# Kernel tuning notes

Hardware: AMD Instinct MI355X
Metric: run time of the kernel (lower is better)

The kernel has to match this reference:

```python
import jax, jax.numpy as jnp
import numpy as np

NEG = jnp.float32(-1e9)
N_PRE = 12000   # n_train_pre_nms (module default training=True)
N_POST = 2000   # n_train_post_nms
MIN_SIZE = 16.0
NMS_THRESH = 0.7


def _make_anchors(feat_size=64, stride=16):
    scales = np.array([128.0, 256.0, 512.0])
    ratios = np.array([0.5, 1.0, 2.0])
    ws = (scales[:, None] * np.sqrt(1.0 / ratios)[None, :]).reshape(-1)  # [9]
    hs = (scales[:, None] * np.sqrt(ratios)[None, :]).reshape(-1)        # [9]
    ctr = (np.arange(feat_size) + 0.5) * stride
    cy, cx = np.meshgrid(ctr, ctr, indexing='ij')
    cx = cx.reshape(-1, 1); cy = cy.reshape(-1, 1)                       # [4096,1]
    x1 = cx - 0.5 * ws[None, :]; y1 = cy - 0.5 * hs[None, :]
    x2 = cx + 0.5 * ws[None, :]; y2 = cy + 0.5 * hs[None, :]
    return np.stack([x1, y1, x2, y2], axis=-1).reshape(-1, 4).astype(np.float32)  # [36864,4]


def setup_inputs() -> dict:
    key = jax.random.key(0)
    k1, k2 = jax.random.split(key)
    anchors = jnp.asarray(_make_anchors())[None]            # [1, 36864, 4]
    B, N = 8, anchors.shape[1]
    pred_loc = jax.random.normal(k1, (B, N, 4), jnp.float32) * 0.2
    pred_obj = jax.random.normal(k2, (B, N, 2), jnp.float32)
    return {"img_height": 1024, "img_width": 1024,
            "anchor_boxes": anchors, "pred_loc": pred_loc, "pred_obj": pred_obj}


def _decode(anchors, loc, img_w, img_h):
    # anchors [N,4] (x1,y1,x2,y2), loc [N,4] (dx,dy,dw,dh)
    w = anchors[:, 2] - anchors[:, 0]
    h = anchors[:, 3] - anchors[:, 1]
    cx = anchors[:, 0] + 0.5 * w
    cy = anchors[:, 1] + 0.5 * h
    pcx = loc[:, 0] * w + cx
    pcy = loc[:, 1] * h + cy
    pw = jnp.exp(loc[:, 2]) * w
    ph = jnp.exp(loc[:, 3]) * h
    x1 = jnp.clip(pcx - 0.5 * pw, 0.0, img_w)
    y1 = jnp.clip(pcy - 0.5 * ph, 0.0, img_h)
    x2 = jnp.clip(pcx + 0.5 * pw, 0.0, img_w)
    y2 = jnp.clip(pcy + 0.5 * ph, 0.0, img_h)
    return jnp.stack([x1, y1, x2, y2], axis=-1)  # [N,4]


def _iou_one_vs_all(box, boxes):
    # box [4], boxes [M,4]
    ix1 = jnp.maximum(box[0], boxes[:, 0])
    iy1 = jnp.maximum(box[1], boxes[:, 1])
    ix2 = jnp.minimum(box[2], boxes[:, 2])
    iy2 = jnp.minimum(box[3], boxes[:, 3])
    inter = jnp.maximum(ix2 - ix1, 0.0) * jnp.maximum(iy2 - iy1, 0.0)
    a0 = (box[2] - box[0]) * (box[3] - box[1])
    a1 = (boxes[:, 2] - boxes[:, 0]) * (boxes[:, 3] - boxes[:, 1])
    return inter / jnp.maximum(a0 + a1 - inter, 1e-9)


def _greedy_nms(boxes, scores):
    # boxes [M,4], scores [M] (invalid entries already NEG). Selects the first
    # N_POST boxes kept by greedy IoU suppression (exactly torchvision nms +
    # [:n_post] truncation, since greedy NMS emits in descending-score order).
    def step(s, _):
        i = jnp.argmax(s)
        valid = s[i] > NEG * 0.5
        box = boxes[i]
        suppress = _iou_one_vs_all(box, boxes) > NMS_THRESH  # includes self
        s = jnp.where(suppress, NEG, s)
        return s, (box, valid)
    _, (kept, mask) = jax.lax.scan(step, scores, None, length=N_POST)
    return jnp.where(mask[:, None], kept, 0.0), mask  # [N_POST,4], [N_POST]


def reference(img_height, img_width, anchor_boxes, pred_loc, pred_obj):
    img_h = jnp.float32(img_height)
    img_w = jnp.float32(img_width)
    anchors = anchor_boxes[0]                                    # [N,4]
    scores = jax.nn.softmax(pred_obj, axis=2)[:, :, 1]           # [B,N]
    boxes = jax.vmap(lambda l: _decode(anchors, l, img_w, img_h))(pred_loc)  # [B,N,4]
    # min-size filter -> mask scores instead of dynamic filtering
    valid = jnp.all(boxes[..., 2:] - boxes[..., :2] >= MIN_SIZE, axis=-1)    # [B,N]
    scores = jnp.where(valid, scores, NEG)
    # descending sort + pre-NMS truncation == top_k
    top_s, top_i = jax.lax.top_k(scores, N_PRE)                  # [B,N_PRE]
    top_boxes = jnp.take_along_axis(boxes, top_i[..., None], axis=1)         # [B,N_PRE,4]
    kept_boxes, kept_mask = jax.vmap(_greedy_nms)(top_boxes, top_s)
    return kept_boxes, kept_mask  # [B,N_POST,4] padded, [B,N_POST] validity
```

## Files before the change

### kernel.cpp

```cpp
#include <hip/hip_runtime.h>

typedef unsigned long long u64;
typedef unsigned int u32;

#define B_SZ   8
#define N_ANC  36864
#define N_PRE  12000
#define N_POST 2000
#define SEG    2048
#define NSEG   6
#define MAXC   (SEG * NSEG)
#define NW     (SEG / 64)
#define NDW    (MAXC / 64)
#define NBLK   144

__device__ __forceinline__ float area_of(float4 p) {
  return __fmul_rn(__fsub_rn(p.z, p.x), __fsub_rn(p.w, p.y));
}

__device__ __forceinline__ bool iou_gt_a(float4 p, float4 q, float a0, float a1) {
  float ix1 = fmaxf(p.x, q.x), iy1 = fmaxf(p.y, q.y);
  float ix2 = fminf(p.z, q.z), iy2 = fminf(p.w, q.w);
  float iw = fmaxf(__fsub_rn(ix2, ix1), 0.0f);
  float ih = fmaxf(__fsub_rn(iy2, iy1), 0.0f);
  float inter = __fmul_rn(iw, ih);
  float den = fmaxf(__fsub_rn(__fadd_rn(a0, a1), inter), 1e-9f);
  return (inter / den) > 0.7f;
}

__device__ __forceinline__ void block_sync_lgkm() {
  __builtin_amdgcn_sched_barrier(0);
  asm volatile("s_waitcnt lgkmcnt(0)" ::: "memory");
  __builtin_amdgcn_s_barrier();
  __builtin_amdgcn_sched_barrier(0);
}

__global__ __launch_bounds__(256) void k_decode(
    const int* __restrict__ imh_p, const int* __restrict__ imw_p,
    const float* __restrict__ anchors, const float* __restrict__ loc,
    const float* __restrict__ obj, float4* __restrict__ boxes,
    u64* __restrict__ keys, u32* __restrict__ hist)
{
  __shared__ u32 lh[2048];
  int t = threadIdx.x;
#pragma unroll
  for (int i = 0; i < 8; ++i) lh[t + i * 256] = 0;
  __syncthreads();

  int n = blockIdx.x * 256 + t;
  int b = blockIdx.y;
  float a0 = anchors[n * 4 + 0], a1 = anchors[n * 4 + 1];
  float a2 = anchors[n * 4 + 2], a3 = anchors[n * 4 + 3];
  size_t off = (size_t)b * N_ANC + n;
  float l0 = loc[off * 4 + 0], l1 = loc[off * 4 + 1];
  float l2 = loc[off * 4 + 2], l3 = loc[off * 4 + 3];

  float w  = __fsub_rn(a2, a0);
  float h  = __fsub_rn(a3, a1);
  float cx = __fadd_rn(a0, __fmul_rn(0.5f, w));
  float cy = __fadd_rn(a1, __fmul_rn(0.5f, h));
  float pcx = __fadd_rn(__fmul_rn(l0, w), cx);
  float pcy = __fadd_rn(__fmul_rn(l1, h), cy);
  float pw  = __fmul_rn(expf(l2), w);
  float ph  = __fmul_rn(expf(l3), h);
  float imw = (float)imw_p[0], imh = (float)imh_p[0];
  float hx = __fmul_rn(0.5f, pw), hy = __fmul_rn(0.5f, ph);
  float x1 = fminf(fmaxf(__fsub_rn(pcx, hx), 0.0f), imw);
  float y1 = fminf(fmaxf(__fsub_rn(pcy, hy), 0.0f), imh);
  float x2 = fminf(fmaxf(__fadd_rn(pcx, hx), 0.0f), imw);
  float y2 = fminf(fmaxf(__fadd_rn(pcy, hy), 0.0f), imh);
  boxes[off] = make_float4(x1, y1, x2, y2);

  bool valid = (__fsub_rn(x2, x1) >= 16.0f) && (__fsub_rn(y2, y1) >= 16.0f);

  float o0 = obj[off * 2 + 0], o1 = obj[off * 2 + 1];
  float m  = fmaxf(o0, o1);
  float e0 = expf(__fsub_rn(o0, m));
  float e1 = expf(__fsub_rn(o1, m));
  float s  = e1 / __fadd_rn(e0, e1);
  float sc = valid ? s : -1e9f;

  u32 u  = __float_as_uint(sc);
  u32 fk = (u & 0x80000000u) ? ~u : (u | 0x80000000u);
  u32 sk = ~fk;
  u64 key = ((u64)sk << 32) | (u32)n;
  keys[off] = key;
  atomicAdd(&lh[(u32)(key >> 53)], 1u);
  __syncthreads();
#pragma unroll
  for (int i = 0; i < 8; ++i) {
    u32 v = lh[t + i * 256];
    if (v) atomicAdd(&hist[b * 2048 + t + i * 256], v);
  }
}

__global__ __launch_bounds__(256) void k_pick1(
    const u32* __restrict__ hist, u32* __restrict__ T1, u32* __restrict__ Base1)
{
  int b = blockIdx.x, t = threadIdx.x;
  const u32* h = hist + b * 2048;
  __shared__ u32 part[256], pre[256];
  u32 loc[8], s = 0;
#pragma unroll
  for (int i = 0; i < 8; ++i) { loc[i] = h[t * 8 + i]; s += loc[i]; }
  part[t] = s;
  __syncthreads();
  if (t == 0) { u32 acc = 0; for (int i = 0; i < 256; ++i) { pre[i] = acc; acc += part[i]; } }
  __syncthreads();
  u32 acc = pre[t];
#pragma unroll
  for (int i = 0; i < 8; ++i) {
    u32 na = acc + loc[i];
    if (acc < N_PRE && na >= N_PRE) { T1[b] = (u32)(t * 8 + i); Base1[b] = acc; }
    acc = na;
  }
}

__global__ __launch_bounds__(256) void k_hist2(
    const u64* __restrict__ keys, const u32* __restrict__ T1,
    u32* __restrict__ hist)
{
  int b = blockIdx.y;
  u32 t1 = T1[b];
  __shared__ u32 lh[2048];
  int t = threadIdx.x;
#pragma unroll
  for (int i = 0; i < 8; ++i) lh[t + i * 256] = 0;
  __syncthreads();
#pragma unroll
  for (int k = 0; k < 4; ++k) {
    int i = blockIdx.x * 1024 + k * 256 + t;
    u64 key = keys[(size_t)b * N_ANC + i];
    if ((u32)(key >> 53) == t1) atomicAdd(&lh[(u32)(key >> 42) & 0x7FFu], 1u);
  }
  __syncthreads();
#pragma unroll
  for (int i = 0; i < 8; ++i) {
    u32 v = lh[t + i * 256];
    if (v) atomicAdd(&hist[b * 2048 + t + i * 256], v);
  }
}

__global__ __launch_bounds__(256) void k_pick2(
    const u32* __restrict__ hist, const u32* __restrict__ T1,
    const u32* __restrict__ Base1, u32* __restrict__ T2)
{
  int b = blockIdx.x, t = threadIdx.x;
  const u32* h = hist + b * 2048;
  __shared__ u32 part[256], pre[256];
  u32 loc[8], s = 0;
#pragma unroll
  for (int i = 0; i < 8; ++i) { loc[i] = h[t * 8 + i]; s += loc[i]; }
  part[t] = s;
  __syncthreads();
  if (t == 0) { u32 acc = Base1[b]; for (int i = 0; i < 256; ++i) { pre[i] = acc; acc += part[i]; } }
  __syncthreads();
  u32 acc = pre[t];
#pragma unroll
  for (int i = 0; i < 8; ++i) {
    u32 na = acc + loc[i];
    if (acc < N_PRE && na >= N_PRE) T2[b] = (T1[b] << 11) | (u32)(t * 8 + i);
    acc = na;
  }
}

__global__ __launch_bounds__(256) void k_count(
    const u64* __restrict__ keys, const u32* __restrict__ T2,
    u32* __restrict__ bcnt)
{
  int b = blockIdx.y;
  int i = blockIdx.x * 256 + threadIdx.x;
  u64 key = keys[(size_t)b * N_ANC + i];
  bool pred = (u32)(key >> 42) <= T2[b];
  u64 bal = __ballot(pred);
  __shared__ u32 wc[4];
  int wv = threadIdx.x >> 6, lane = threadIdx.x & 63;
  if (lane == 0) wc[wv] = (u32)__popcll(bal);
  __syncthreads();
  if (threadIdx.x == 0)
    bcnt[b * NBLK + blockIdx.x] = wc[0] + wc[1] + wc[2] + wc[3];
}

__global__ __launch_bounds__(256) void k_scatter(
    const u64* __restrict__ keys, const u32* __restrict__ T2,
    const u32* __restrict__ bcnt, u64* __restrict__ cand)
{
  int b = blockIdx.y, bx = blockIdx.x;
  int t = threadIdx.x;
  __shared__ u32 cnts[NBLK];
  __shared__ u32 wc[4];
  __shared__ u32 sbase;
  if (t < NBLK) cnts[t] = bcnt[b * NBLK + t];
  u64 key = keys[(size_t)b * N_ANC + bx * 256 + t];
  bool pred = (u32)(key >> 42) <= T2[b];
  u64 bal = __ballot(pred);
  int wv = t >> 6, lane = t & 63;
  if (lane == 0) wc[wv] = (u32)__popcll(bal);
  __syncthreads();
  if (t == 0) { u32 a = 0; for (int i = 0; i < bx; ++i) a += cnts[i]; sbase = a; }
  __syncthreads();
  u32 base = sbase;
  for (int w = 0; w < wv; ++w) base += wc[w];
  u32 rank = (u32)__popcll(bal & ((1ull << lane) - 1ull));
  if (pred) {
    u32 pos = base + rank;
    if (pos < MAXC) cand[(size_t)b * MAXC + pos] = key;
  }
}

#define SIDX(x) ((x) + ((x) >> 5))
__global__ __launch_bounds__(1024) void k_sort_tile(u64* __restrict__ a)
{
  int b = blockIdx.y, base = blockIdx.x * 2048;
  u64* p = a + (size_t)b * MAXC + base;
  __shared__ u64 lds[2048 + 64];
  int t = threadIdx.x;
  lds[SIDX(t)] = p[t];
  lds[SIDX(t + 1024)] = p[t + 1024];
  __syncthreads();
  for (int k = 2; k <= 2048; k <<= 1) {
    for (int j = k >> 1; j > 0; j >>= 1) {
      int i = ((t & ~(j - 1)) << 1) | (t & (j - 1));
      int l = i | j;
      bool asc = ((i & k) == 0);
      u64 x = lds[SIDX(i)], y = lds[SIDX(l)];
      if ((x > y) == asc) { lds[SIDX(i)] = y; lds[SIDX(l)] = x; }
      __syncthreads();
    }
  }
  p[t] = lds[SIDX(t)];
  p[t + 1024] = lds[SIDX(t + 1024)];
}

__global__ __launch_bounds__(256) void k_merge_gather(
    const u64* __restrict__ cand, const float4* __restrict__ boxes,
    float4* __restrict__ gbox, u64* __restrict__ deadm)
{
  int b = blockIdx.y;
  int p = blockIdx.x * 256 + threadIdx.x;
  const u64* cb = cand + (size_t)b * MAXC;
  u64 key = cb[p];
  int r = p >> 11;
  int rank = p & 2047;
#pragma unroll
  for (int s = 0; s < NSEG; ++s) {
    if (s == r) continue;
    const u64* run = cb + (s << 11);
    int lo = 0;
#pragma unroll
    for (int step = 2048; step >= 1; step >>= 1) {
      int np = lo + step;
      if (np <= 2048 && run[np - 1] < key) lo = np;
    }
    rank += lo;
  }
  bool valid = ((u32)(key >> 32) < 0x80000000u) && (rank < N_PRE);
  float4 bx = make_float4(0.f, 0.f, 0.f, 0.f);
  if (valid) bx = boxes[(size_t)b * N_ANC + (u32)key];
  gbox[(size_t)b * MAXC + rank] = bx;
  if (!valid) atomicOr(&deadm[b * NDW + (rank >> 6)], 1ull << (rank & 63));
}

template <int NWAVES>
__device__ __forceinline__ void segmask_tile_body(
    int b, int sg, int tile, const float4* __restrict__ gbox,
    u64* smask, u64* smaskT)
{
  __shared__ float4 rbox[64];
  __shared__ float rarea[64];
  __shared__ u64 diag[64];
  int r = tile, rg = 0;
  while (r >= 32 - rg) { r -= 32 - rg; ++rg; }
  int cw = rg + r;
  const float4* gb = gbox + (size_t)b * MAXC + sg * SEG;
  int t = threadIdx.x;
  if (t < 64) { float4 bx = gb[rg * 64 + t]; rbox[t] = bx; rarea[t] = area_of(bx); }
  __syncthreads();
  int wv = t >> 6, lane = t & 63;
  const int RPW = 64 / NWAVES;
  u64* srow = smask + (size_t)(b * NSEG + sg) * SEG * NW + (size_t)rg * 64 * NW;
  float4 cb4 = gb[cw * 64 + lane];
  float ca = area_of(cb4);
  bool isdiag = (cw == rg);
  for (int rr = wv * RPW; rr < wv * RPW + RPW; ++rr) {
    bool p = iou_gt_a(rbox[rr], cb4, rarea[rr], ca);
    if (isdiag) p = p && (lane > rr);
    u64 m = __ballot(p);
    if (lane == 0) { srow[(size_t)rr * NW + cw] = m; if (isdiag) diag[rr] = m; }
  }
  if (isdiag) {
    __syncthreads();
    if (t < 64) {
      u64 s = 0;
      for (int q = 0; q < 64; ++q) s |= ((diag[q] >> t) & 1ull) << q;
      smaskT[(size_t)(b * NSEG + sg) * SEG + rg * 64 + t] = s;
    }
  }
}

__global__ __launch_bounds__(256) void k_segmask0(
    const float4* __restrict__ gbox, u64* __restrict__ smask,
    u64* __restrict__ smaskT)
{
  segmask_tile_body<4>(blockIdx.y, 0, blockIdx.x, gbox, smask, smaskT);
}

__global__ __launch_bounds__(256) void k_cross(
    const float4* __restrict__ gbox, const float4* __restrict__ keptb,
    const int* __restrict__ meta, u64* __restrict__ deadm, int sg)
{
  int b = blockIdx.y;
  if (meta[b * 8 + 1]) return;
  __shared__ float4 kb[256]; __shared__ float ka[256];
  int kc = blockIdx.x >> 3, cbk = blockIdx.x & 7;
  int nkept = meta[b * 8 + 0];
  int kbase = kc * 256;
  if (kbase >= nkept) return;
  int kcnt = min(256, nkept - kbase);
  int t = threadIdx.x;
  if (t < kcnt) {
    float4 k4 = keptb[(size_t)b * SEG + kbase + t];
    kb[t] = k4; ka[t] = area_of(k4);
  }
  __syncthreads();
  int gi = sg * SEG + cbk * 256 + t;
  float4 my = gbox[(size_t)b * MAXC + gi];
  float ma = area_of(my);
  bool sup = false;
  for (int kk = 0; kk < kcnt; ++kk) {
    if (iou_gt_a(kb[kk], my, ka[kk], ma)) { sup = true; break; }
  }
  u64 bm = __ballot(sup);
  if ((t & 63) == 0 && bm) atomicOr(&deadm[b * NDW + (gi >> 6)], bm);
}

__device__ void walk_body(
    int b, int sg, const float4* __restrict__ gbox, const u64* smask,
    const u64* smaskT, const u64* __restrict__ deadm,
    int* __restrict__ meta, float4* __restrict__ keptb,
    float* __restrict__ out)
{
  int t = threadIdx.x, wv = t >> 6, lane = t & 63;

  __shared__ u64 rowbuf[2][2048];
  __shared__ u64 stbuf[2][64];
  __shared__ float4 bbox[2][64];
  __shared__ u64 sdead[2];
  __shared__ u32 remv[64];
  __shared__ u32 klist[64];
  __shared__ int s_stop, s_nkept, s_kcnt;

  const u64* smb = smask + (size_t)(b * NSEG + sg) * SEG * NW;
  const u64* stb = smaskT + (size_t)(b * NSEG + sg) * SEG;
  const u64* dmb = deadm + b * NDW + sg * NW;
  const float4* gb = gbox + (size_t)b * MAXC + sg * SEG;
  float4* kbuf = keptb + (size_t)b * SEG;
  float4* ob = (float4*)(out + (size_t)b * N_POST * 4);
  float* om = out + (size_t)B_SZ * N_POST * 4 + (size_t)b * N_POST;

  {
    u64 a = smb[t], c = smb[t + 1024];
    u64 st_ = 0; float4 bb_ = make_float4(0.f, 0.f, 0.f, 0.f);
    if (t < 64) { st_ = stb[t]; bb_ = gb[t]; }
    u64 sd_ = (t == 0) ? dmb[0] : 0;
    rowbuf[0][t] = a;
    rowbuf[0][t + 1024] = c;
    if (t < 64) { stbuf[0][t] = st_; bbox[0][t] = bb_; remv[t] = 0; }
    if (t == 0) { sdead[0] = sd_; s_stop = 0; s_nkept = meta[b * 8 + 0]; }
  }
  int p0 = t - 64, p1 = p0 + 960, p2 = p0 + 1920;
  u64 ra = 0, rc = 0, re = 0, rst = 0, rsd = 0;
  float4 rbb = make_float4(0.f, 0.f, 0.f, 0.f);
  if (wv > 0) {
    const u64* src = smb + 2048;
    ra = src[p0];
    rc = src[p1];
    if (p0 < 128) re = src[p2];
    if (p0 < 64) { rst = stb[64 + p0]; rbb = gb[64 + p0]; }
    if (t == 64) rsd = dmb[1];
  }
  block_sync_lgkm();

  for (int g = 0; g < NW; ++g) {
    int cb = g & 1, nb = cb ^ 1;
    if (wv > 0) {
      if (g < NW - 1) {
        rowbuf[nb][p0] = ra;
        rowbuf[nb][p1] = rc;
        if (p0 < 128) rowbuf[nb][p2] = re;
        if (p0 < 64) { stbuf[nb][p0] = rst; bbox[nb][p0] = rbb; }
        if (t == 64) sdead[nb] = rsd;
      }
      if (g < NW - 2) {
        const u64* src = smb + (size_t)(g + 2) * 2048;
        ra = src[p0];
        rc = src[p1];
        if (p0 < 128) re = src[p2];
        if (p0 < 64) { rst = stb[(g + 2) * 64 + p0]; rbb = gb[(g + 2) * 64 + p0]; }
        if (t == 64) rsd = dmb[g + 2];
      }
    } else {
      int l = lane;
      u64 S = stbuf[cb][l];
      u64 remg = ((u64)remv[2 * g + 1] << 32) | remv[2 * g];
      u64 avail = ~(remg | sdead[cb]);
      u64 km = 0;
      while (avail) {
        bool al = (avail >> l) & 1;
        u64 newk = __ballot(al && (S & avail) == 0ull);
        u64 nd   = __ballot(al && (S & newk) != 0ull);
        km |= newk;
        avail &= ~(newk | nd);
      }
      int nk0 = s_nkept;
      int rem = N_POST - nk0;
      int kc = __popcll(km);
      bool stop = (kc >= rem);
      int rank = __popcll(km & ((1ull << l) - 1ull));
      if (((km >> l) & 1) && rank < rem) {
        float4 bx = bbox[cb][l];
        kbuf[nk0 + rank] = bx;
        ob[nk0 + rank] = bx;
        om[nk0 + rank] = 1.0f;
        klist[rank] = (u32)l;
      }
      if (l == 0) {
        int eff = stop ? rem : kc;
        s_kcnt = eff;
        s_nkept = nk0 + eff;
        if (stop) s_stop = 1;
      }
    }
    block_sync_lgkm();
    if (s_stop) break;
    if (g < NW - 1) {
      int kcnt = s_kcnt;
      if (kcnt) {
        u32* rb32 = (u32*)rowbuf[cb];
        for (int i = t; i < kcnt * 64; i += 1024) {
          int kk = i >> 6, w = i & 63;
          if ((w >> 1) > g) {
            u32 v = rb32[klist[kk] * 64 + w];
            if (v) atomicOr(&remv[w], v);
          }
        }
      }
    }
    block_sync_lgkm();
  }
  int nk = s_nkept;
  bool fin = s_stop || (sg == NSEG - 1);
  if (t == 0) { meta[b * 8 + 0] = nk; if (fin) meta[b * 8 + 1] = 1; }
  if (fin) {
    float4 zero = make_float4(0.f, 0.f, 0.f, 0.f);
    for (int i = nk + t; i < N_POST; i += 1024) { ob[i] = zero; om[i] = 0.0f; }
  }
}

__global__ __launch_bounds__(1024) void k_walkmask(
    const float4* __restrict__ gbox, u64* smask, u64* smaskT,
    const u64* __restrict__ deadm, int* __restrict__ meta,
    float4* __restrict__ keptb, float* __restrict__ out, int sg, int msg)
{
  int b = blockIdx.y;
  if (blockIdx.x == 0) {
    if (meta[b * 8 + 1]) return;
    walk_body(b, sg, gbox, smask, smaskT, deadm, meta, keptb, out);
  } else {
    if (msg < 0 || msg >= NSEG) return;
    if (meta[b * 8 + 1]) return;
    segmask_tile_body<16>(b, msg, blockIdx.x - 1, gbox, smask, smaskT);
  }
}

extern "C" void kernel_launch(void* const* d_in, const int* in_sizes, int n_in,
                              void* d_out, int out_size, void* d_ws, size_t ws_size,
                              hipStream_t stream)
{
  const int*   imh     = (const int*)d_in[0];
  const int*   imw     = (const int*)d_in[1];
  const float* anchors = (const float*)d_in[2];
  const float* loc     = (const float*)d_in[3];
  const float* obj     = (const float*)d_in[4];
  float* out = (float*)d_out;

  char* ws = (char*)d_ws;
  size_t off = 0;
  float4* boxes = (float4*)(ws + off); off += (size_t)B_SZ * N_ANC * 16;
  u64*    keys  = (u64*)   (ws + off); off += (size_t)B_SZ * N_ANC * 8;
  u64*    cand  = (u64*)   (ws + off); off += (size_t)B_SZ * MAXC * 8;
  float4* gbox  = (float4*)(ws + off); off += (size_t)B_SZ * MAXC * 16;
  float4* keptb = (float4*)(ws + off); off += (size_t)B_SZ * SEG * 16;
  off = (off + 255) & ~(size_t)255;
  char*   zr    = ws + off;
  u32*    hist1 = (u32*)(zr);
  u32*    hist2 = (u32*)(zr + 65536);
  u32*    T1    = (u32*)(zr + 131072);
  u32*    Base1 = (u32*)(zr + 131072 + 32);
  u32*    T2    = (u32*)(zr + 131072 + 64);
  int*    meta  = (int*)(zr + 131072 + 128);
  u64*    deadm = (u64*)(zr + 131072 + 128 + 256);
  u32*    bcnt  = (u32*)(zr + 131072 + 128 + 256 + (size_t)B_SZ * NDW * 8);
  size_t  zr_sz = 131072 + 128 + 256 + (size_t)B_SZ * NDW * 8
                + (size_t)B_SZ * NBLK * 4;
  off += (zr_sz + 255) & ~(size_t)255;
  u64*    smask  = (u64*)(ws + off); off += (size_t)B_SZ * NSEG * SEG * NW * 8;
  u64*    smaskT = (u64*)(ws + off); off += (size_t)B_SZ * NSEG * SEG * 8;

  hipMemsetAsync(zr, 0, zr_sz, stream);
  hipMemsetAsync(cand, 0xFF, (size_t)B_SZ * MAXC * 8, stream);

  k_decode<<<dim3(NBLK, B_SZ), 256, 0, stream>>>(imh, imw, anchors, loc, obj,
                                                 boxes, keys, hist1);
  k_pick1<<<B_SZ, 256, 0, stream>>>(hist1, T1, Base1);
  k_hist2<<<dim3(36, B_SZ), 256, 0, stream>>>(keys, T1, hist2);
  k_pick2<<<B_SZ, 256, 0, stream>>>(hist2, T1, Base1, T2);

  k_count<<<dim3(NBLK, B_SZ), 256, 0, stream>>>(keys, T2, bcnt);
  k_scatter<<<dim3(NBLK, B_SZ), 256, 0, stream>>>(keys, T2, bcnt, cand);

  k_sort_tile<<<dim3(NSEG, B_SZ), 1024, 0, stream>>>(cand);
  k_merge_gather<<<dim3(MAXC / 256, B_SZ), 256, 0, stream>>>(cand, boxes, gbox, deadm);

  k_segmask0<<<dim3(528, B_SZ), 256, 0, stream>>>(gbox, smask, smaskT);

  k_walkmask<<<dim3(529, B_SZ), 1024, 0, stream>>>(gbox, smask, smaskT, deadm,
                                                   meta, keptb, out, 0, 1);
  for (int sg = 1; sg < NSEG; ++sg) {
    k_cross<<<dim3(64, B_SZ), 256, 0, stream>>>(gbox, keptb, meta, deadm, sg);
    int msg = (sg + 1 < NSEG) ? sg + 1 : -1;
    int gx = (msg >= 0) ? 529 : 1;
    k_walkmask<<<dim3(gx, B_SZ), 1024, 0, stream>>>(gbox, smask, smaskT, deadm,
                                                    meta, keptb, out, sg, msg);
  }
}
```

Before: 240.4 us.

## Skip second radix pass when possible, skip dead tiles in IoU mask, plain syncs

k_pick1 now checks whether the whole threshold bin fits in the candidate buffer. If it does, it sets T2 directly and the second histogram and pick kernels exit early. The segment-mask tile routine skips IoU work for column tiles that are entirely dead and for dead rows. It also loads row boxes into registers instead of shared memory, which removes a block barrier. The custom lgkm-wait barrier is replaced with __syncthreads. Including the whole threshold bin can admit extra candidates beyond N_PRE, which relies on later rank validity checks.

Result: slower. 254.1 us (+5.7%).

```diff
diff --git a/kernel.cpp b/kernel.cpp
--- a/kernel.cpp
+++ b/kernel.cpp
@@ -26,13 +26,6 @@
   float inter = __fmul_rn(iw, ih);
   float den = fmaxf(__fsub_rn(__fadd_rn(a0, a1), inter), 1e-9f);
   return (inter / den) > 0.7f;
-}
-
-__device__ __forceinline__ void block_sync_lgkm() {
-  __builtin_amdgcn_sched_barrier(0);
-  asm volatile("s_waitcnt lgkmcnt(0)" ::: "memory");
-  __builtin_amdgcn_s_barrier();
-  __builtin_amdgcn_sched_barrier(0);
 }
 
 __global__ __launch_bounds__(256) void k_decode(
@@ -95,7 +88,8 @@
 }
 
 __global__ __launch_bounds__(256) void k_pick1(
-    const u32* __restrict__ hist, u32* __restrict__ T1, u32* __restrict__ Base1)
+    const u32* __restrict__ hist, u32* __restrict__ T1, u32* __restrict__ Base1,
+    u32* __restrict__ T2, u32* __restrict__ need2)
 {
   int b = blockIdx.x, t = threadIdx.x;
   const u32* h = hist + b * 2048;
@@ -111,16 +105,22 @@
 #pragma unroll
   for (int i = 0; i < 8; ++i) {
     u32 na = acc + loc[i];
-    if (acc < N_PRE && na >= N_PRE) { T1[b] = (u32)(t * 8 + i); Base1[b] = acc; }
+    if (acc < N_PRE && na >= N_PRE) {
+      u32 bin = (u32)(t * 8 + i);
+      T1[b] = bin; Base1[b] = acc;
+      if (na <= MAXC) T2[b] = (bin << 11) | 0x7FFu;
+      else need2[b] = 1;
+    }
     acc = na;
   }
 }
 
 __global__ __launch_bounds__(256) void k_hist2(
     const u64* __restrict__ keys, const u32* __restrict__ T1,
-    u32* __restrict__ hist)
+    const u32* __restrict__ need2, u32* __restrict__ hist)
 {
   int b = blockIdx.y;
+  if (!need2[b]) return;
   u32 t1 = T1[b];
   __shared__ u32 lh[2048];
   int t = threadIdx.x;
@@ -143,9 +143,11 @@
 
 __global__ __launch_bounds__(256) void k_pick2(
     const u32* __restrict__ hist, const u32* __restrict__ T1,
-    const u32* __restrict__ Base1, u32* __restrict__ T2)
+    const u32* __restrict__ Base1, const u32* __restrict__ need2,
+    u32* __restrict__ T2)
 {
   int b = blockIdx.x, t = threadIdx.x;
+  if (!need2[b]) return;
   const u32* h = hist + b * 2048;
   __shared__ u32 part[256], pre[256];
   u32 loc[8], s = 0;
@@ -262,31 +264,53 @@
 }
 
 template <int NWAVES>
-__device__ __forceinline__ void segmask_tile_body(
+__device__ __forceinline__ void segmask_tile_v3(
     int b, int sg, int tile, const float4* __restrict__ gbox,
-    u64* smask, u64* smaskT)
-{
-  __shared__ float4 rbox[64];
-  __shared__ float rarea[64];
-  __shared__ u64 diag[64];
+    const u64* __restrict__ deadm,
+    u64* __restrict__ smask, u64* __restrict__ smaskT, u64* diag)
+{
+  const int RPW = 64 / NWAVES;
   int r = tile, rg = 0;
   while (r >= 32 - rg) { r -= 32 - rg; ++rg; }
   int cw = rg + r;
   const float4* gb = gbox + (size_t)b * MAXC + sg * SEG;
-  int t = threadIdx.x;
-  if (t < 64) { float4 bx = gb[rg * 64 + t]; rbox[t] = bx; rarea[t] = area_of(bx); }
-  __syncthreads();
-  int wv = t >> 6, lane = t & 63;
-  const int RPW = 64 / NWAVES;
+  const u64* dmb = deadm + b * NDW + sg * NW;
+  int t = threadIdx.x, wv = t >> 6, lane = t & 63;
+  int rbase = rg * 64 + wv * RPW;
+  bool isdiag = (cw == rg);
+  u64 rowdead = dmb[rg];
+  u64 coldead = dmb[cw];
   u64* srow = smask + (size_t)(b * NSEG + sg) * SEG * NW + (size_t)rg * 64 * NW;
-  float4 cb4 = gb[cw * 64 + lane];
-  float ca = area_of(cb4);
-  bool isdiag = (cw == rg);
-  for (int rr = wv * RPW; rr < wv * RPW + RPW; ++rr) {
-    bool p = iou_gt_a(rbox[rr], cb4, rarea[rr], ca);
-    if (isdiag) p = p && (lane > rr);
-    u64 m = __ballot(p);
-    if (lane == 0) { srow[(size_t)rr * NW + cw] = m; if (isdiag) diag[rr] = m; }
+
+  if (coldead == ~0ull) {
+    if (lane == 0) {
+#pragma unroll
+      for (int i = 0; i < RPW; ++i) {
+        int rr = wv * RPW + i;
+        srow[(size_t)rr * NW + cw] = 0;
+        if (isdiag) diag[rr] = 0;
+      }
+    }
+  } else {
+    float4 rb[RPW];
+#pragma unroll
+    for (int i = 0; i < RPW; ++i) rb[i] = gb[rbase + i];
+    float ra[RPW];
+#pragma unroll
+    for (int i = 0; i < RPW; ++i) ra[i] = area_of(rb[i]);
+    float4 cb4 = gb[cw * 64 + lane];
+    float ca = area_of(cb4);
+#pragma unroll
+    for (int i = 0; i < RPW; ++i) {
+      int rr = wv * RPW + i;
+      u64 m = 0;
+      if (!((rowdead >> rr) & 1)) {
+        bool p = iou_gt_a(rb[i], cb4, ra[i], ca);
+        if (isdiag) p = p && (lane > rr);
+        m = __ballot(p);
+      }
+      if (lane == 0) { srow[(size_t)rr * NW + cw] = m; if (isdiag) diag[rr] = m; }
+    }
   }
   if (isdiag) {
     __syncthreads();
@@ -298,11 +322,12 @@
   }
 }
 
-__global__ __launch_bounds__(256) void k_segmask0(
-    const float4* __restrict__ gbox, u64* __restrict__ smask,
-    u64* __restrict__ smaskT)
-{
-  segmask_tile_body<4>(blockIdx.y, 0, blockIdx.x, gbox, smask, smaskT);
+__global__ __launch_bounds__(256) void k_segmask(
+    const float4* __restrict__ gbox, const u64* __restrict__ deadm,
+    u64* __restrict__ smask, u64* __restrict__ smaskT, int sg)
+{
+  __shared__ u64 diag[64];
+  segmask_tile_v3<4>(blockIdx.y, sg, blockIdx.x, gbox, deadm, smask, smaskT, diag);
 }
 
 __global__ __launch_bounds__(256) void k_cross(
@@ -379,7 +404,7 @@
     if (p0 < 64) { rst = stb[64 + p0]; rbb = gb[64 + p0]; }
     if (t == 64) rsd = dmb[1];
   }
-  block_sync_lgkm();
+  __syncthreads();
 
   for (int g = 0; g < NW; ++g) {
     int cb = g & 1, nb = cb ^ 1;
@@ -431,7 +456,7 @@
         if (stop) s_stop = 1;
       }
     }
-    block_sync_lgkm();
+    __syncthreads();
     if (s_stop) break;
     if (g < NW - 1) {
       int kcnt = s_kcnt;
@@ -446,7 +471,7 @@
         }
       }
     }
-    block_sync_lgkm();
+    __syncthreads();
   }
   int nk = s_nkept;
   bool fin = s_stop || (sg == NSEG - 1);
@@ -462,14 +487,14 @@
     const u64* __restrict__ deadm, int* __restrict__ meta,
     float4* __restrict__ keptb, float* __restrict__ out, int sg, int msg)
 {
+  __shared__ u64 diag[64];
   int b = blockIdx.y;
+  if (meta[b * 8 + 1]) return;
   if (blockIdx.x == 0) {
-    if (meta[b * 8 + 1]) return;
     walk_body(b, sg, gbox, smask, smaskT, deadm, meta, keptb, out);
   } else {
     if (msg < 0 || msg >= NSEG) return;
-    if (meta[b * 8 + 1]) return;
-    segmask_tile_body<16>(b, msg, blockIdx.x - 1, gbox, smask, smaskT);
+    segmask_tile_v3<16>(b, msg, blockIdx.x - 1, gbox, deadm, smask, smaskT, diag);
   }
 }
 
@@ -498,6 +523,7 @@
   u32*    T1    = (u32*)(zr + 131072);
   u32*    Base1 = (u32*)(zr + 131072 + 32);
   u32*    T2    = (u32*)(zr + 131072 + 64);
+  u32*    need2 = (u32*)(zr + 131072 + 96);
   int*    meta  = (int*)(zr + 131072 + 128);
   u64*    deadm = (u64*)(zr + 131072 + 128 + 256);
   u32*    bcnt  = (u32*)(zr + 131072 + 128 + 256 + (size_t)B_SZ * NDW * 8);
@@ -512,9 +538,9 @@
 
   k_decode<<<dim3(NBLK, B_SZ), 256, 0, stream>>>(imh, imw, anchors, loc, obj,
                                                  boxes, keys, hist1);
-  k_pick1<<<B_SZ, 256, 0, stream>>>(hist1, T1, Base1);
-  k_hist2<<<dim3(36, B_SZ), 256, 0, stream>>>(keys, T1, hist2);
-  k_pick2<<<B_SZ, 256, 0, stream>>>(hist2, T1, Base1, T2);
+  k_pick1<<<B_SZ, 256, 0, stream>>>(hist1, T1, Base1, T2, need2);
+  k_hist2<<<dim3(36, B_SZ), 256, 0, stream>>>(keys, T1, need2, hist2);
+  k_pick2<<<B_SZ, 256, 0, stream>>>(hist2, T1, Base1, need2, T2);
 
   k_count<<<dim3(NBLK, B_SZ), 256, 0, stream>>>(keys, T2, bcnt);
   k_scatter<<<dim3(NBLK, B_SZ), 256, 0, stream>>>(keys, T2, bcnt, cand);
@@ -522,7 +548,7 @@
   k_sort_tile<<<dim3(NSEG, B_SZ), 1024, 0, stream>>>(cand);
   k_merge_gather<<<dim3(MAXC / 256, B_SZ), 256, 0, stream>>>(cand, boxes, gbox, deadm);
 
-  k_segmask0<<<dim3(528, B_SZ), 256, 0, stream>>>(gbox, smask, smaskT);
+  k_segmask<<<dim3(528, B_SZ), 256, 0, stream>>>(gbox, deadm, smask, smaskT, 0);
 
   k_walkmask<<<dim3(529, B_SZ), 1024, 0, stream>>>(gbox, smask, smaskT, deadm,
                                                    meta, keptb, out, 0, 1);
```
